# Kernel tuning notes

Hardware: AMD Instinct MI355X
Metric: run time of the kernel (lower is better)

## Reference

```python
import jax, jax.numpy as jnp
import numpy as np

B, S, NE = 4096, 128, 2
H = 64  # lstm hidden

def setup_inputs() -> dict:
    key = jax.random.key(0)
    ks = jax.random.split(key, 12)
    d = {
        'self_obs':     jax.random.normal(ks[0], (B, S, 15), jnp.float32),
        'teammate_obs': jax.random.normal(ks[1], (B, S, 13), jnp.float32),
        'enemy_obs':    jax.random.normal(ks[2], (B, S, NE, 13), jnp.float32),
        'next_cp_obs':  jax.random.normal(ks[3], (B, S, 6), jnp.float32),
        'W1':  jax.random.normal(ks[4], (47, 256), jnp.float32) * 0.1,
        'b1':  jnp.zeros((256,), jnp.float32),
        'W2':  jax.random.normal(ks[5], (256, 128), jnp.float32) * 0.1,
        'b2':  jnp.zeros((128,), jnp.float32),
        'Wih': jax.random.normal(ks[6], (128, 4 * H), jnp.float32) * 0.1,
        'bih': jnp.zeros((4 * H,), jnp.float32),
        'Whh': jax.random.normal(ks[7], (H, 4 * H), jnp.float32) * 0.1,
        'bhh': jnp.zeros((4 * H,), jnp.float32),
        'Wv':  jax.random.normal(ks[8], (H, 1), jnp.float32) * 0.1,
        'bv':  jnp.zeros((1,), jnp.float32),
    }
    return d

def reference(self_obs, teammate_obs, enemy_obs, next_cp_obs,
              W1, b1, W2, b2, Wih, bih, Whh, bhh, Wv, bv):
    # enemy pooling + concat -> [B,S,47]
    en_mean = enemy_obs.mean(axis=2)
    x = jnp.concatenate([self_obs, teammate_obs, en_mean, next_cp_obs], axis=2)
    # MLP encoder -> [B,S,128]
    emb = jax.nn.relu(jax.nn.relu(x @ W1 + b1) @ W2 + b2)
    # precompute input projection for all timesteps -> [B,S,4H]
    wx = emb @ Wih + bih
    h0 = jnp.zeros((B, H), wx.dtype)
    c0 = jnp.zeros((B, H), wx.dtype)

    def step(carry, wx_t):
        h, c = carry
        gates = wx_t + h @ Whh + bhh          # [B,4H]
        i, f, g, o = jnp.split(gates, 4, axis=-1)
        i = jax.nn.sigmoid(i)
        f = jax.nn.sigmoid(f)
        g = jnp.tanh(g)
        o = jax.nn.sigmoid(o)
        c = f * c + i * g
        h = o * jnp.tanh(c)
        return (h, c), h

    (hn, cn), outs = jax.lax.scan(step, (h0, c0), jnp.swapaxes(wx, 0, 1))
    out = jnp.swapaxes(outs, 0, 1)            # [B,S,H]
    val = (out @ Wv + bv).reshape(B, S, 1)
    return val, hn[None], cn[None]
```

## Files before the change

### kernel.cpp

```cpp
#include <hip/hip_runtime.h>

#define BB 4096
#define SS 128
#define NB 16
#define NT 256

typedef __attribute__((ext_vector_type(8))) short short8;
typedef __attribute__((ext_vector_type(4))) float f32x4;
typedef unsigned short ushort_t;
typedef unsigned int uint_t;

#define SX_STR   72
#define SH1_STR  264
#define SEMB_STR 136
#define SH_STR   72
#define ENC_LDS_USHORTS (32 * SH1_STR + 32 * SEMB_STR)

__device__ __forceinline__ ushort_t f2bf(float f) {
    union { float f; unsigned u; } x; x.f = f;
    unsigned r = x.u + 0x7FFFu + ((x.u >> 16) & 1u);
    return (ushort_t)(r >> 16);
}
__device__ __forceinline__ uint_t pack2(float a, float b) {
    return (uint_t)f2bf(a) | ((uint_t)f2bf(b) << 16);
}
__device__ __forceinline__ float bflo(uint_t u) {
    union { unsigned u; float f; } x; x.u = u << 16; return x.f;
}
__device__ __forceinline__ float bfhi(uint_t u) {
    union { unsigned u; float f; } x; x.u = u & 0xFFFF0000u; return x.f;
}
__device__ __forceinline__ float bf2f(ushort_t h) {
    union { unsigned u; float f; } x; x.u = ((unsigned)h) << 16; return x.f;
}
__device__ __forceinline__ float fsig(float x) {
    return __builtin_amdgcn_rcpf(1.f + __expf(-x));
}
__device__ __forceinline__ float ftanh(float x) {
    return 1.f - 2.f * __builtin_amdgcn_rcpf(__expf(2.f * x) + 1.f);
}
__device__ __forceinline__ void barrier_lgkm() {
    asm volatile("s_waitcnt lgkmcnt(0)\n\ts_barrier" ::: "memory");
}

union FragU { short8 v; ushort_t u[8]; };

__global__ void podcritic_prep(const float* __restrict__ W1, const float* __restrict__ W2,
                               const float* __restrict__ Wih, const float* __restrict__ Whh,
                               short8* __restrict__ img)
{
    const int W = blockIdx.x * 4 + (threadIdx.x >> 6);
    const int l = threadIdx.x & 63;
    const int q = l >> 4, m = l & 15;
    FragU u;
    #pragma unroll
    for (int j = 0; j < 8; ++j) {
        float v;
        if (W < 32)       { int nt = W >> 1,        kk = W & 1;        int k = kk*32 + q*8 + j;
                            v = (k < 47) ? W1[k*256 + nt*16 + m] : 0.f; }
        else if (W < 96)  { int f = W - 32, nt = f >> 3, kk = f & 7;   int k = kk*32 + q*8 + j;
                            v = W2[k*128 + nt*16 + m]; }
        else if (W < 160) { int f = W - 96, nt = f >> 2, kk = f & 3;   int k = kk*32 + q*8 + j;
                            v = Wih[k*256 + nt*16 + m]; }
        else              { int f = W - 160, nt = f >> 1, kk = f & 1;  int k = kk*32 + q*8 + j;
                            v = Whh[k*256 + nt*16 + m]; }
        u.u[j] = f2bf(v);
    }
    img[W * 64 + l] = u.v;
}

__device__ __forceinline__ void enc_block(
    ushort_t* smem,
    const float* __restrict__ self_obs, const float* __restrict__ tm_obs,
    const float* __restrict__ en_obs,   const float* __restrict__ cp_obs,
    const float* __restrict__ b1, const float* __restrict__ b2,
    const float* __restrict__ bih, const float* __restrict__ bhh,
    const short8* __restrict__ img, uint_t* __restrict__ wx, int c0, int e)
{
    ushort_t* sh1 = smem;
    ushort_t* sxe = smem + 32 * SH1_STR;

    const int t = threadIdx.x;
    const int w = t >> 6, l = t & 63, q = l >> 4, m = l & 15;
    const int bg = e & 255, b0 = bg * NB;
    const int ytile = e >> 8;
    const int sbase = c0 + ytile * 2;

    {
        const int col = t & 63, rw0 = t >> 6;
        const float* p; int stride, soff; float scale;
        if (col < 15)      { p = self_obs + col;      stride = 15; soff = 0;  scale = 0.5f; }
        else if (col < 28) { p = tm_obs + (col - 15); stride = 13; soff = 0;  scale = 0.5f; }
        else if (col < 41) { p = en_obs + (col - 28); stride = 26; soff = 13; scale = 0.5f; }
        else if (col < 47) { p = cp_obs + (col - 41); stride = 6;  soff = 0;  scale = 0.5f; }
        else               { p = self_obs;            stride = 0;  soff = 0;  scale = 0.f; }
        #pragma unroll
        for (int jj = 0; jj < 8; ++jj) {
            int rr = 4 * jj + rw0;
            int mt = rr >> 4, r = rr & 15;
            int bs = (b0 + r) * SS + sbase + mt;
            int o = bs * stride;
            float v = scale * (p[o] + p[o + soff]);
            sxe[rr * SX_STR + col] = f2bf(v);
        }
    }
    float bias1[4], bias2[2], bgf[4];
    #pragma unroll
    for (int i = 0; i < 4; ++i) bias1[i] = b1[w * 64 + i * 16 + m];
    #pragma unroll
    for (int i = 0; i < 2; ++i) bias2[i] = b2[32 * w + 16 * i + m];
    #pragma unroll
    for (int i = 0; i < 4; ++i) { int n = (w + 4 * i) * 16 + m; bgf[i] = bih[n] + bhh[n]; }
    barrier_lgkm();

    {
        short8 w1f[4][2];
        #pragma unroll
        for (int i = 0; i < 4; ++i)
            #pragma unroll
            for (int kk = 0; kk < 2; ++kk)
                w1f[i][kk] = img[(((4 * w + i) * 2) + kk) * 64 + l];
        f32x4 c1[2][4];
        #pragma unroll
        for (int mt = 0; mt < 2; ++mt)
            #pragma unroll
            for (int i = 0; i < 4; ++i)
                c1[mt][i] = (f32x4){bias1[i], bias1[i], bias1[i], bias1[i]};
        #pragma unroll
        for (int kk = 0; kk < 2; ++kk) {
            #pragma unroll
            for (int mt = 0; mt < 2; ++mt) {
                short8 a = *(const short8*)&sxe[(mt * 16 + m) * SX_STR + kk * 32 + q * 8];
                #pragma unroll
                for (int i = 0; i < 4; ++i)
                    c1[mt][i] = __builtin_amdgcn_mfma_f32_16x16x32_bf16(a, w1f[i][kk], c1[mt][i], 0, 0, 0);
            }
        }
        #pragma unroll
        for (int mt = 0; mt < 2; ++mt)
            #pragma unroll
            for (int i = 0; i < 4; ++i) {
                int col = w * 64 + i * 16 + m;
                #pragma unroll
                for (int r = 0; r < 4; ++r)
                    sh1[(mt * 16 + q * 4 + r) * SH1_STR + col] = f2bf(fmaxf(c1[mt][i][r], 0.f));
            }
    }
    barrier_lgkm();

    {
        short8 w2f[2][8];
        #pragma unroll
        for (int i = 0; i < 2; ++i)
            #pragma unroll
            for (int kk = 0; kk < 8; ++kk)
                w2f[i][kk] = img[(32 + ((2 * w + i) * 8) + kk) * 64 + l];
        f32x4 c2[2][2];
        #pragma unroll
        for (int mt = 0; mt < 2; ++mt)
            #pragma unroll
            for (int i = 0; i < 2; ++i)
                c2[mt][i] = (f32x4){bias2[i], bias2[i], bias2[i], bias2[i]};
        #pragma unroll
        for (int kk = 0; kk < 8; ++kk) {
            #pragma unroll
            for (int mt = 0; mt < 2; ++mt) {
                short8 a = *(const short8*)&sh1[(mt * 16 + m) * SH1_STR + kk * 32 + q * 8];
                #pragma unroll
                for (int i = 0; i < 2; ++i)
                    c2[mt][i] = __builtin_amdgcn_mfma_f32_16x16x32_bf16(a, w2f[i][kk], c2[mt][i], 0, 0, 0);
            }
        }
        #pragma unroll
        for (int mt = 0; mt < 2; ++mt)
            #pragma unroll
            for (int i = 0; i < 2; ++i) {
                int col = 32 * w + 16 * i + m;
                #pragma unroll
                for (int r = 0; r < 4; ++r)
                    sxe[(mt * 16 + q * 4 + r) * SEMB_STR + col] = f2bf(fmaxf(c2[mt][i][r], 0.f));
            }
    }
    barrier_lgkm();

    {
        short8 wihf[4][4];
        #pragma unroll
        for (int i = 0; i < 4; ++i)
            #pragma unroll
            for (int kk = 0; kk < 4; ++kk)
                wihf[i][kk] = img[(96 + ((w + 4 * i) * 4) + kk) * 64 + l];
        #pragma unroll
        for (int mt = 0; mt < 2; ++mt) {
            f32x4 g[4];
            #pragma unroll
            for (int i = 0; i < 4; ++i) g[i] = (f32x4){bgf[i], bgf[i], bgf[i], bgf[i]};
            #pragma unroll
            for (int kk = 0; kk < 4; ++kk) {
                short8 a = *(const short8*)&sxe[(mt * 16 + m) * SEMB_STR + kk * 32 + q * 8];
                #pragma unroll
                for (int i = 0; i < 4; ++i)
                    g[i] = __builtin_amdgcn_mfma_f32_16x16x32_bf16(a, wihf[i][kk], g[i], 0, 0, 0);
            }
            int slc = ytile * 2 + mt;
            uint_t* dst = wx + (size_t)(slc * 256 + bg) * 2048 + l * 2;
            #pragma unroll
            for (int i = 0; i < 4; ++i) {
                uint2 vv;
                vv.x = pack2(g[i][0], g[i][1]);
                vv.y = pack2(g[i][2], g[i][3]);
                *(uint2*)(dst + (w + 4 * i) * 128) = vv;
            }
        }
    }
}

__device__ __forceinline__ void rec_block(
    ushort_t* smem,
    const short8* __restrict__ whhimg, const uint_t* __restrict__ wx,
    ushort_t* __restrict__ hws, float* __restrict__ cws,
    ushort_t* __restrict__ hseq, float* __restrict__ out,
    int first, int last, int csr)
{
    const int t = threadIdx.x;
    const int w = t >> 6, l = t & 63, q = l >> 4, m = l & 15;
    const int bg = blockIdx.x, b0 = bg * NB;

    short8 whhf[4][2];
    #pragma unroll
    for (int a = 0; a < 4; ++a)
        #pragma unroll
        for (int kk = 0; kk < 2; ++kk)
            whhf[a][kk] = whhimg[(((w + 4 * a) * 2) + kk) * 64 + l];

    float creg[4], hlast[4] = {0.f, 0.f, 0.f, 0.f};
    if (first) {
        #pragma unroll
        for (int r = 0; r < 4; ++r) creg[r] = 0.f;
        int idx4 = t * 4, row = idx4 >> 6, col = idx4 & 63;
        uint2 z; z.x = 0u; z.y = 0u;
        *(uint2*)&smem[row * SH_STR + col] = z;
    } else {
        int idx4 = t * 4, row = idx4 >> 6, col = idx4 & 63;
        uint2 hv2 = *(const uint2*)((const uint_t*)(hws + (size_t)bg * 1024 + idx4));
        *(uint2*)&smem[row * SH_STR + col] = hv2;
        float4 cv = *(const float4*)(cws + ((size_t)bg * 256 + t) * 4);
        creg[0] = cv.x; creg[1] = cv.y; creg[2] = cv.z; creg[3] = cv.w;
    }

    uint2 upf[2][4];
    {
        const uint_t* p0 = wx + (size_t)(0 * 256 + bg) * 2048 + l * 2;
        const uint_t* p1 = wx + (size_t)(1 * 256 + bg) * 2048 + l * 2;
        #pragma unroll
        for (int a = 0; a < 4; ++a) {
            upf[0][a] = *(const uint2*)(p0 + (w + 4 * a) * 128);
            upf[1][a] = *(const uint2*)(p1 + (w + 4 * a) * 128);
        }
    }
    ushort_t* hsp = hseq + (size_t)(b0 + q * 4) * 64 + 16 * w + m;
    const size_t hstep = (size_t)BB * 64;

    barrier_lgkm();

    #define REC_STEP(PAR, SLV)                                                          \
    do {                                                                                \
        const int sl_ = (SLV);                                                          \
        ushort_t* shc = smem + (PAR) * (NB * SH_STR);                                   \
        ushort_t* shn = smem + (1 - (PAR)) * (NB * SH_STR);                             \
        short8 af0 = *(const short8*)&shc[m * SH_STR + q * 8];                          \
        short8 af1 = *(const short8*)&shc[m * SH_STR + 32 + q * 8];                     \
        f32x4 g[4];                                                                     \
        _Pragma("unroll")                                                               \
        for (int a = 0; a < 4; ++a) {                                                   \
            g[a][0] = bflo(upf[PAR][a].x); g[a][1] = bfhi(upf[PAR][a].x);               \
            g[a][2] = bflo(upf[PAR][a].y); g[a][3] = bfhi(upf[PAR][a].y);               \
        }                                                                               \
        {                                                                               \
            int snext = (sl_ + 2 < csr) ? (sl_ + 2) : sl_;                              \
            const uint_t* pn = wx + (size_t)(snext * 256 + bg) * 2048 + l * 2;          \
            _Pragma("unroll")                                                           \
            for (int a = 0; a < 4; ++a)                                                 \
                upf[PAR][a] = *(const uint2*)(pn + (w + 4 * a) * 128);                  \
        }                                                                               \
        _Pragma("unroll")                                                               \
        for (int a = 0; a < 4; ++a) {                                                   \
            g[a] = __builtin_amdgcn_mfma_f32_16x16x32_bf16(af0, whhf[a][0], g[a], 0, 0, 0); \
            g[a] = __builtin_amdgcn_mfma_f32_16x16x32_bf16(af1, whhf[a][1], g[a], 0, 0, 0); \
        }                                                                               \
        _Pragma("unroll")                                                               \
        for (int r = 0; r < 4; ++r) {                                                   \
            float gi = fsig(g[0][r]);                                                   \
            float gf = fsig(g[1][r]);                                                   \
            float gg = ftanh(g[2][r]);                                                  \
            float go = fsig(g[3][r]);                                                   \
            float c  = gf * creg[r] + gi * gg;                                          \
            creg[r] = c;                                                                \
            float h = go * ftanh(c);                                                    \
            hlast[r] = h;                                                               \
            ushort_t hb = f2bf(h);                                                      \
            shn[(q * 4 + r) * SH_STR + 16 * w + m] = hb;                                \
            hsp[(size_t)sl_ * hstep + r * 64] = hb;                                     \
        }                                                                               \
        barrier_lgkm();                                                                 \
    } while (0)

    for (int sl = 0; sl < csr; sl += 2) {
        REC_STEP(0, sl);
        REC_STEP(1, sl + 1);
    }
    #undef REC_STEP

    if (!last) {
        const int jcol = 16 * w + m;
        #pragma unroll
        for (int r = 0; r < 4; ++r)
            hws[(size_t)bg * 1024 + (q * 4 + r) * 64 + jcol] = f2bf(hlast[r]);
        float4 cv; cv.x = creg[0]; cv.y = creg[1]; cv.z = creg[2]; cv.w = creg[3];
        *(float4*)(cws + ((size_t)bg * 256 + t) * 4) = cv;
    } else {
        const int jcol = 16 * w + m;
        #pragma unroll
        for (int r = 0; r < 4; ++r) {
            int row = b0 + q * 4 + r;
            out[BB * SS + (size_t)row * 64 + jcol]           = hlast[r];
            out[BB * SS + BB * 64 + (size_t)row * 64 + jcol] = creg[r];
        }
    }
}

__device__ __forceinline__ void val_block(
    const ushort_t* __restrict__ hseq, const float* __restrict__ Wv,
    const float* __restrict__ bv, float* __restrict__ out, int c0, int vb)
{
    const int t = threadIdx.x;
    const int row = vb * 256 + t;
    const ushort_t* hp = hseq + (size_t)row * 64;
    float pv = bv[0];
    #pragma unroll
    for (int k = 0; k < 8; ++k) {
        uint4 hv = *(const uint4*)(hp + k * 8);
        float4 w0 = *(const float4*)(Wv + k * 8);
        float4 w1 = *(const float4*)(Wv + k * 8 + 4);
        pv += bflo(hv.x) * w0.x + bfhi(hv.x) * w0.y
            + bflo(hv.y) * w0.z + bfhi(hv.y) * w0.w
            + bflo(hv.z) * w1.x + bfhi(hv.z) * w1.y
            + bflo(hv.w) * w1.z + bfhi(hv.w) * w1.w;
    }
    int sl = row >> 12, b = row & 4095;
    out[(size_t)b * SS + c0 + sl] = pv;
}

__global__ __launch_bounds__(NT, 4)
void podcritic_step(const float* __restrict__ self_obs, const float* __restrict__ tm_obs,
                    const float* __restrict__ en_obs,   const float* __restrict__ cp_obs,
                    const float* __restrict__ b1, const float* __restrict__ b2,
                    const float* __restrict__ bih, const float* __restrict__ bhh,
                    const short8* __restrict__ img,
                    uint_t* __restrict__ wx_enc, const uint_t* __restrict__ wx_rec,
                    ushort_t* __restrict__ hws, float* __restrict__ cws,
                    ushort_t* __restrict__ hseq_rec, const ushort_t* __restrict__ hseq_val,
                    const float* __restrict__ Wv, const float* __restrict__ bv,
                    float* __restrict__ out,
                    int enc_c0, int val_c0, int nrec, int nenc, int first, int last, int csr)
{
    __shared__ __align__(16) ushort_t smem[ENC_LDS_USHORTS];
    const int bid = blockIdx.x;
    if (bid < nrec) {
        rec_block(smem, img + 160 * 64, wx_rec, hws, cws, hseq_rec, out, first, last, csr);
    } else if (bid < nrec + nenc) {
        enc_block(smem, self_obs, tm_obs, en_obs, cp_obs, b1, b2, bih, bhh,
                  img, wx_enc, enc_c0, bid - nrec);
    } else {
        val_block(hseq_val, Wv, bv, out, val_c0, bid - nrec - nenc);
    }
}

__global__ __launch_bounds__(NT, 1)
void podcritic_mfma(const float* __restrict__ self_obs,
                    const float* __restrict__ tm_obs,
                    const float* __restrict__ en_obs,
                    const float* __restrict__ cp_obs,
                    const float* __restrict__ W1, const float* __restrict__ b1,
                    const float* __restrict__ W2, const float* __restrict__ b2,
                    const float* __restrict__ Wih, const float* __restrict__ bih,
                    const float* __restrict__ Whh, const float* __restrict__ bhh,
                    const float* __restrict__ Wv, const float* __restrict__ bv,
                    float* __restrict__ out)
{
    __shared__ __align__(16) ushort_t sx[2][NB * SX_STR];
    __shared__ __align__(16) ushort_t sh1[NB * SH1_STR];
    __shared__ __align__(16) ushort_t semb[NB * SEMB_STR];
    __shared__ __align__(16) ushort_t sh[NB * SH_STR];
    __shared__ float sWv[64];

    const int t  = threadIdx.x;
    const int w  = t >> 6;
    const int l  = t & 63;
    const int q  = l >> 4;
    const int m  = l & 15;
    const int b0 = blockIdx.x * NB;

    short8 w1f[4][2];
    short8 w2f[2][8];
    short8 wihf[4][4];
    short8 whhf[4][2];
    float bias1[4], bias2[2], bg[4];

    #pragma unroll
    for (int i = 0; i < 4; ++i) {
        int n = w * 64 + i * 16 + m;
        bias1[i] = b1[n];
        #pragma unroll
        for (int kk = 0; kk < 2; ++kk) {
            FragU u;
            #pragma unroll
            for (int j = 0; j < 8; ++j) {
                int k = kk * 32 + q * 8 + j;
                u.u[j] = f2bf(k < 47 ? W1[k * 256 + n] : 0.f);
            }
            w1f[i][kk] = u.v;
        }
    }
    #pragma unroll
    for (int i = 0; i < 2; ++i) {
        int n = 32 * w + i * 16 + m;
        bias2[i] = b2[n];
        #pragma unroll
        for (int kk = 0; kk < 8; ++kk) {
            FragU u;
            #pragma unroll
            for (int j = 0; j < 8; ++j) {
                int k = kk * 32 + q * 8 + j;
                u.u[j] = f2bf(W2[k * 128 + n]);
            }
            w2f[i][kk] = u.v;
        }
    }
    #pragma unroll
    for (int i = 0; i < 4; ++i) {
        int n = (w + 4 * i) * 16 + m;
        bg[i] = bih[n] + bhh[n];
        #pragma unroll
        for (int kk = 0; kk < 4; ++kk) {
            FragU u;
            #pragma unroll
            for (int j = 0; j < 8; ++j) {
                int k = kk * 32 + q * 8 + j;
                u.u[j] = f2bf(Wih[k * 256 + n]);
            }
            wihf[i][kk] = u.v;
        }
        #pragma unroll
        for (int kk = 0; kk < 2; ++kk) {
            FragU u;
            #pragma unroll
            for (int j = 0; j < 8; ++j) {
                int k = kk * 32 + q * 8 + j;
                u.u[j] = f2bf(Whh[k * 256 + n]);
            }
            whhf[i][kk] = u.v;
        }
    }
    const float bvv = bv[0];
    if (t < 64) sWv[t] = Wv[t];

    for (int idx = t; idx < NB * SH_STR; idx += NT) sh[idx] = 0;

    const int pcol = t & 63;
    const int prow = t >> 6;
    #pragma unroll
    for (int j = 0; j < 4; ++j) {
        int r  = 4 * j + prow;
        int bs = (b0 + r) * SS + 0;
        float v = 0.f;
        if (pcol < 15)      v = self_obs[bs * 15 + pcol];
        else if (pcol < 28) v = tm_obs[bs * 13 + (pcol - 15)];
        else if (pcol < 41) { int kk = pcol - 28;
                              v = 0.5f * (en_obs[(bs * 2) * 13 + kk] + en_obs[(bs * 2) * 13 + 13 + kk]); }
        else if (pcol < 47) v = cp_obs[bs * 6 + (pcol - 41)];
        sx[0][r * SX_STR + pcol] = f2bf(v);
    }
    __syncthreads();

    float creg[4] = {0.f, 0.f, 0.f, 0.f};
    float hreg[4] = {0.f, 0.f, 0.f, 0.f};
    int cur = 0;

    for (int s = 0; s < SS; ++s) {
        float pf[4];
        #pragma unroll
        for (int j = 0; j < 4; ++j) {
            float v = 0.f;
            if (s + 1 < SS) {
                int r  = 4 * j + prow;
                int bs = (b0 + r) * SS + (s + 1);
                if (pcol < 15)      v = self_obs[bs * 15 + pcol];
                else if (pcol < 28) v = tm_obs[bs * 13 + (pcol - 15)];
                else if (pcol < 41) { int kk = pcol - 28;
                                      v = 0.5f * (en_obs[(bs * 2) * 13 + kk] + en_obs[(bs * 2) * 13 + 13 + kk]); }
                else if (pcol < 47) v = cp_obs[bs * 6 + (pcol - 41)];
            }
            pf[j] = v;
        }

        {
            f32x4 c1[4] = {{0,0,0,0},{0,0,0,0},{0,0,0,0},{0,0,0,0}};
            #pragma unroll
            for (int kk = 0; kk < 2; ++kk) {
                short8 a = *(const short8*)&sx[cur][m * SX_STR + kk * 32 + q * 8];
                #pragma unroll
                for (int i = 0; i < 4; ++i)
                    c1[i] = __builtin_amdgcn_mfma_f32_16x16x32_bf16(a, w1f[i][kk], c1[i], 0, 0, 0);
            }
            #pragma unroll
            for (int i = 0; i < 4; ++i) {
                int col = w * 64 + i * 16 + m;
                #pragma unroll
                for (int r = 0; r < 4; ++r)
                    sh1[(q * 4 + r) * SH1_STR + col] = f2bf(fmaxf(c1[i][r] + bias1[i], 0.f));
            }
        }
        __syncthreads();

        {
            f32x4 c2[2] = {{0,0,0,0},{0,0,0,0}};
            #pragma unroll
            for (int kk = 0; kk < 8; ++kk) {
                short8 a = *(const short8*)&sh1[m * SH1_STR + kk * 32 + q * 8];
                #pragma unroll
                for (int i = 0; i < 2; ++i)
                    c2[i] = __builtin_amdgcn_mfma_f32_16x16x32_bf16(a, w2f[i][kk], c2[i], 0, 0, 0);
            }
            #pragma unroll
            for (int i = 0; i < 2; ++i) {
                int col = 32 * w + i * 16 + m;
                #pragma unroll
                for (int r = 0; r < 4; ++r)
                    semb[(q * 4 + r) * SEMB_STR + col] = f2bf(fmaxf(c2[i][r] + bias2[i], 0.f));
            }
        }
        __syncthreads();

        {
            f32x4 g[4];
            #pragma unroll
            for (int i = 0; i < 4; ++i) g[i] = (f32x4){bg[i], bg[i], bg[i], bg[i]};
            #pragma unroll
            for (int kk = 0; kk < 4; ++kk) {
                short8 a = *(const short8*)&semb[m * SEMB_STR + kk * 32 + q * 8];
                #pragma unroll
                for (int i = 0; i < 4; ++i)
                    g[i] = __builtin_amdgcn_mfma_f32_16x16x32_bf16(a, wihf[i][kk], g[i], 0, 0, 0);
            }
            #pragma unroll
            for (int kk = 0; kk < 2; ++kk) {
                short8 a = *(const short8*)&sh[m * SH_STR + kk * 32 + q * 8];
                #pragma unroll
                for (int i = 0; i < 4; ++i)
                    g[i] = __builtin_amdgcn_mfma_f32_16x16x32_bf16(a, whhf[i][kk], g[i], 0, 0, 0);
            }
            const int jcol = 16 * w + m;
            #pragma unroll
            for (int r = 0; r < 4; ++r) {
                float gi = fsig(g[0][r]);
                float gf = fsig(g[1][r]);
                float gg = ftanh(g[2][r]);
                float go = fsig(g[3][r]);
                float c  = gf * creg[r] + gi * gg;
                creg[r] = c;
                float h = go * ftanh(c);
                hreg[r] = h;
                sh[(q * 4 + r) * SH_STR + jcol] = f2bf(h);
            }
            #pragma unroll
            for (int j = 0; j < 4; ++j) {
                int r = 4 * j + prow;
                sx[cur ^ 1][r * SX_STR + pcol] = f2bf(pf[j]);
            }
        }
        __syncthreads();

        {
            int r = t >> 4, pp = t & 15;
            const ushort_t* hp = &sh[r * SH_STR + pp * 4];
            float pv = 0.f;
            #pragma unroll
            for (int j = 0; j < 4; ++j) pv += bf2f(hp[j]) * sWv[pp * 4 + j];
            pv += __shfl_xor(pv, 1, 16);
            pv += __shfl_xor(pv, 2, 16);
            pv += __shfl_xor(pv, 4, 16);
            pv += __shfl_xor(pv, 8, 16);
            if (pp == 0) out[(b0 + r) * SS + s] = pv + bvv;
        }
        cur ^= 1;
    }

    {
        const int jcol = 16 * w + m;
        #pragma unroll
        for (int r = 0; r < 4; ++r) {
            int row = b0 + q * 4 + r;
            out[BB * SS + row * 64 + jcol]           = hreg[r];
            out[BB * SS + BB * 64 + row * 64 + jcol] = creg[r];
        }
    }
}

extern "C" void kernel_launch(void* const* d_in, const int* in_sizes, int n_in,
                              void* d_out, int out_size, void* d_ws, size_t ws_size,
                              hipStream_t stream) {
    const float* self_obs = (const float*)d_in[0];
    const float* tm_obs   = (const float*)d_in[1];
    const float* en_obs   = (const float*)d_in[2];
    const float* cp_obs   = (const float*)d_in[3];
    const float* W1  = (const float*)d_in[4];
    const float* b1  = (const float*)d_in[5];
    const float* W2  = (const float*)d_in[6];
    const float* b2  = (const float*)d_in[7];
    const float* Wih = (const float*)d_in[8];
    const float* bih = (const float*)d_in[9];
    const float* Whh = (const float*)d_in[10];
    const float* bhh = (const float*)d_in[11];
    const float* Wv  = (const float*)d_in[12];
    const float* bv  = (const float*)d_in[13];
    float* out = (float*)d_out;

    const size_t h_bytes   = 256 * 1024 * 2;
    const size_t c_bytes   = 256 * 1024 * 4;
    const size_t img_bytes = 192 * 64 * 16;

    const int CSr = 16, NCHr = 8;
    const size_t wx_chunk   = (size_t)CSr * 256 * 2048 * 4;
    const size_t hseq_chunk = (size_t)CSr * BB * 64 * 2;
    const size_t need = 2 * wx_chunk + h_bytes + c_bytes + img_bytes + 2 * hseq_chunk;

    if (ws_size >= need) {
        char* p = (char*)d_ws;
        uint_t*   wxb[2]   = { (uint_t*)p, (uint_t*)(p + wx_chunk) };
        ushort_t* hws      = (ushort_t*)(p + 2 * wx_chunk);
        float*    cws      = (float*)(p + 2 * wx_chunk + h_bytes);
        short8*   img      = (short8*)(p + 2 * wx_chunk + h_bytes + c_bytes);
        ushort_t* hseqb[2] = { (ushort_t*)(p + 2 * wx_chunk + h_bytes + c_bytes + img_bytes),
                               (ushort_t*)(p + 2 * wx_chunk + h_bytes + c_bytes + img_bytes + hseq_chunk) };

        const int nenc_full = 128 * CSr;
        const int nval_full = CSr * BB / 256;

        podcritic_prep<<<48, NT, 0, stream>>>(W1, W2, Wih, Whh, img);

        podcritic_step<<<nenc_full, NT, 0, stream>>>(
            self_obs, tm_obs, en_obs, cp_obs, b1, b2, bih, bhh, img,
            wxb[0], wxb[0], hws, cws, hseqb[0], hseqb[0], Wv, bv, out,
            0, 0, 0, nenc_full, 0, 0, CSr);

        for (int c = 0; c < NCHr; ++c) {
            int nenc = (c + 1 < NCHr) ? nenc_full : 0;
            int nval = (c > 0) ? nval_full : 0;
            int grid = 256 + nenc + nval;
            podcritic_step<<<grid, NT, 0, stream>>>(
                self_obs, tm_obs, en_obs, cp_obs, b1, b2, bih, bhh, img,
                wxb[(c + 1) & 1], wxb[c & 1], hws, cws,
                hseqb[c & 1], hseqb[(c > 0 ? (c - 1) : 0) & 1], Wv, bv, out,
                (c + 1) * CSr, (c - 1) * CSr,
                256, nenc, (c == 0) ? 1 : 0, (c == NCHr - 1) ? 1 : 0, CSr);
        }
        podcritic_step<<<nval_full, NT, 0, stream>>>(
            self_obs, tm_obs, en_obs, cp_obs, b1, b2, bih, bhh, img,
            wxb[0], wxb[0], hws, cws, hseqb[0], hseqb[(NCHr - 1) & 1], Wv, bv, out,
            0, (NCHr - 1) * CSr, 0, 0, 0, 0, CSr);
    } else {
        podcritic_mfma<<<BB / NB, NT, 0, stream>>>(
            self_obs, tm_obs, en_obs, cp_obs,
            W1, b1, W2, b2, Wih, bih, Whh, bhh, Wv, bv, out);
    }
}
```

Measured before the change: 427.7 us.

## Fuse value head into recurrent step and enlarge chunk size

The value projection (h @ Wv + bv) is now computed inside each recurrent step from the LDS copy of h, using a 16-lane shuffle reduction, and written straight to the output. This drops the hseq global buffer, the separate val blocks and the final value launch. With less workspace needed, the host picks 32-step chunks (4 chunks) when the workspace allows, which halves the number of launches. The cost is extra LDS reads and shuffles on the serial recurrence critical path after every barrier.

```diff
diff --git a/kernel.cpp b/kernel.cpp
--- a/kernel.cpp
+++ b/kernel.cpp
@@ -219,12 +219,13 @@
     ushort_t* smem,
     const short8* __restrict__ whhimg, const uint_t* __restrict__ wx,
     ushort_t* __restrict__ hws, float* __restrict__ cws,
-    ushort_t* __restrict__ hseq, float* __restrict__ out,
-    int first, int last, int csr)
+    const float* __restrict__ Wv, const float* __restrict__ bv,
+    float* __restrict__ out, int rc0, int first, int last, int csr)
 {
     const int t = threadIdx.x;
     const int w = t >> 6, l = t & 63, q = l >> 4, m = l & 15;
     const int bg = blockIdx.x, b0 = bg * NB;
+    const int vr = t >> 4, vp = t & 15;
 
     short8 whhf[4][2];
     #pragma unroll
@@ -232,6 +233,9 @@
         #pragma unroll
         for (int kk = 0; kk < 2; ++kk)
             whhf[a][kk] = whhimg[(((w + 4 * a) * 2) + kk) * 64 + l];
+
+    const float4 wv = *(const float4*)(Wv + vp * 4);
+    const float bvv = bv[0];
 
     float creg[4], hlast[4] = {0.f, 0.f, 0.f, 0.f};
     if (first) {
@@ -258,8 +262,6 @@
             upf[1][a] = *(const uint2*)(p1 + (w + 4 * a) * 128);
         }
     }
-    ushort_t* hsp = hseq + (size_t)(b0 + q * 4) * 64 + 16 * w + m;
-    const size_t hstep = (size_t)BB * 64;
 
     barrier_lgkm();
 
@@ -298,11 +300,19 @@
             creg[r] = c;                                                                \
             float h = go * ftanh(c);                                                    \
             hlast[r] = h;                                                               \
-            ushort_t hb = f2bf(h);                                                      \
-            shn[(q * 4 + r) * SH_STR + 16 * w + m] = hb;                                \
-            hsp[(size_t)sl_ * hstep + r * 64] = hb;                                     \
+            shn[(q * 4 + r) * SH_STR + 16 * w + m] = f2bf(h);                           \
         }                                                                               \
         barrier_lgkm();                                                                 \
+        {            \
+            uint2 hv = *(const uint2*)&shn[vr * SH_STR + vp * 4];                       \
+            float pv = bflo(hv.x) * wv.x + bfhi(hv.x) * wv.y                            \
+                     + bflo(hv.y) * wv.z + bfhi(hv.y) * wv.w;                           \
+            pv += __shfl_xor(pv, 1, 16);                                                \
+            pv += __shfl_xor(pv, 2, 16);                                                \
+            pv += __shfl_xor(pv, 4, 16);                                                \
+            pv += __shfl_xor(pv, 8, 16);                                                \
+            if (vp == 0) out[(size_t)(b0 + vr) * SS + rc0 + sl_] = pv + bvv;            \
+        }                                                                               \
     } while (0)
 
     for (int sl = 0; sl < csr; sl += 2) {
@@ -327,28 +337,6 @@
             out[BB * SS + BB * 64 + (size_t)row * 64 + jcol] = creg[r];
         }
     }
-}
-
-__device__ __forceinline__ void val_block(
-    const ushort_t* __restrict__ hseq, const float* __restrict__ Wv,
-    const float* __restrict__ bv, float* __restrict__ out, int c0, int vb)
-{
-    const int t = threadIdx.x;
-    const int row = vb * 256 + t;
-    const ushort_t* hp = hseq + (size_t)row * 64;
-    float pv = bv[0];
-    #pragma unroll
-    for (int k = 0; k < 8; ++k) {
-        uint4 hv = *(const uint4*)(hp + k * 8);
-        float4 w0 = *(const float4*)(Wv + k * 8);
-        float4 w1 = *(const float4*)(Wv + k * 8 + 4);
-        pv += bflo(hv.x) * w0.x + bfhi(hv.x) * w0.y
-            + bflo(hv.y) * w0.z + bfhi(hv.y) * w0.w
-            + bflo(hv.z) * w1.x + bfhi(hv.z) * w1.y
-            + bflo(hv.w) * w1.z + bfhi(hv.w) * w1.w;
-    }
-    int sl = row >> 12, b = row & 4095;
-    out[(size_t)b * SS + c0 + sl] = pv;
 }
 
 __global__ __launch_bounds__(NT, 4)
@@ -359,20 +347,18 @@
                     const short8* __restrict__ img,
                     uint_t* __restrict__ wx_enc, const uint_t* __restrict__ wx_rec,
                     ushort_t* __restrict__ hws, float* __restrict__ cws,
-                    ushort_t* __restrict__ hseq_rec, const ushort_t* __restrict__ hseq_val,
                     const float* __restrict__ Wv, const float* __restrict__ bv,
                     float* __restrict__ out,
-                    int enc_c0, int val_c0, int nrec, int nenc, int first, int last, int csr)
+                    int enc_c0, int rec_c0, int nrec, int first, int last, int csr)
 {
     __shared__ __align__(16) ushort_t smem[ENC_LDS_USHORTS];
     const int bid = blockIdx.x;
     if (bid < nrec) {
-        rec_block(smem, img + 160 * 64, wx_rec, hws, cws, hseq_rec, out, first, last, csr);
-    } else if (bid < nrec + nenc) {
+        rec_block(smem, img + 160 * 64, wx_rec, hws, cws, Wv, bv, out,
+                  rec_c0, first, last, csr);
+    } else {
         enc_block(smem, self_obs, tm_obs, en_obs, cp_obs, b1, b2, bih, bhh,
                   img, wx_enc, enc_c0, bid - nrec);
-    } else {
-        val_block(hseq_val, Wv, bv, out, val_c0, bid - nrec - nenc);
     }
 }
 
@@ -630,45 +616,41 @@
     const size_t c_bytes   = 256 * 1024 * 4;
     const size_t img_bytes = 192 * 64 * 16;
 
-    const int CSr = 16, NCHr = 8;
-    const size_t wx_chunk   = (size_t)CSr * 256 * 2048 * 4;
-    const size_t hseq_chunk = (size_t)CSr * BB * 64 * 2;
-    const size_t need = 2 * wx_chunk + h_bytes + c_bytes + img_bytes + 2 * hseq_chunk;
-
-    if (ws_size >= need) {
+    auto need_for = [&](int cs) -> size_t {
+        size_t wx_chunk = (size_t)cs * 256 * 2048 * 4;
+        return 2 * wx_chunk + h_bytes + c_bytes + img_bytes;
+    };
+
+    int CSr = 0, NCHr = 0;
+    if (ws_size >= need_for(32))      { CSr = 32; NCHr = 4; }
+    else if (ws_size >= need_for(16)) { CSr = 16; NCHr = 8; }
+
+    if (CSr) {
+        const size_t wx_chunk = (size_t)CSr * 256 * 2048 * 4;
         char* p = (char*)d_ws;
-        uint_t*   wxb[2]   = { (uint_t*)p, (uint_t*)(p + wx_chunk) };
-        ushort_t* hws      = (ushort_t*)(p + 2 * wx_chunk);
-        float*    cws      = (float*)(p + 2 * wx_chunk + h_bytes);
-        short8*   img      = (short8*)(p + 2 * wx_chunk + h_bytes + c_bytes);
-        ushort_t* hseqb[2] = { (ushort_t*)(p + 2 * wx_chunk + h_bytes + c_bytes + img_bytes),
-                               (ushort_t*)(p + 2 * wx_chunk + h_bytes + c_bytes + img_bytes + hseq_chunk) };
+        uint_t*   wxb[2] = { (uint_t*)p, (uint_t*)(p + wx_chunk) };
+        ushort_t* hws    = (ushort_t*)(p + 2 * wx_chunk);
+        float*    cws    = (float*)(p + 2 * wx_chunk + h_bytes);
+        short8*   img    = (short8*)(p + 2 * wx_chunk + h_bytes + c_bytes);
 
         const int nenc_full = 128 * CSr;
-        const int nval_full = CSr * BB / 256;
 
         podcritic_prep<<<48, NT, 0, stream>>>(W1, W2, Wih, Whh, img);
 
         podcritic_step<<<nenc_full, NT, 0, stream>>>(
             self_obs, tm_obs, en_obs, cp_obs, b1, b2, bih, bhh, img,
-            wxb[0], wxb[0], hws, cws, hseqb[0], hseqb[0], Wv, bv, out,
-            0, 0, 0, nenc_full, 0, 0, CSr);
+            wxb[0], wxb[0], hws, cws, Wv, bv, out,
+            0, 0, 0, 0, 0, CSr);
 
         for (int c = 0; c < NCHr; ++c) {
             int nenc = (c + 1 < NCHr) ? nenc_full : 0;
-            int nval = (c > 0) ? nval_full : 0;
-            int grid = 256 + nenc + nval;
+            int grid = 256 + nenc;
             podcritic_step<<<grid, NT, 0, stream>>>(
                 self_obs, tm_obs, en_obs, cp_obs, b1, b2, bih, bhh, img,
-                wxb[(c + 1) & 1], wxb[c & 1], hws, cws,
-                hseqb[c & 1], hseqb[(c > 0 ? (c - 1) : 0) & 1], Wv, bv, out,
-                (c + 1) * CSr, (c - 1) * CSr,
-                256, nenc, (c == 0) ? 1 : 0, (c == NCHr - 1) ? 1 : 0, CSr);
-        }
-        podcritic_step<<<nval_full, NT, 0, stream>>>(
-            self_obs, tm_obs, en_obs, cp_obs, b1, b2, bih, bhh, img,
-            wxb[0], wxb[0], hws, cws, hseqb[0], hseqb[(NCHr - 1) & 1], Wv, bv, out,
-            0, (NCHr - 1) * CSr, 0, 0, 0, 0, CSr);
+                wxb[(c + 1) & 1], wxb[c & 1], hws, cws, Wv, bv, out,
+                (c + 1) * CSr, c * CSr,
+                256, (c == 0) ? 1 : 0, (c == NCHr - 1) ? 1 : 0, CSr);
+        }
     } else {
         podcritic_mfma<<<BB / NB, NT, 0, stream>>>(
             self_obs, tm_obs, en_obs, cp_obs,
```

Measured after the change: 393.6 us. -8.0%, faster.
